# Kernel tuning notes

Hardware: AMD Instinct MI355X
Metric: run time of the kernel (lower is better)

## Reference

```python
import jax, jax.numpy as jnp
import numpy as np
from jax import lax

SCOPE = 15
RICKER_WIDTH = 3.0
DAMP = 0.12
MAX_STEPS = 10


def mexican_hat(scope, width, damping):
    # ricker / mexican-hat wavelet sampled at `scope` integer-spaced points, scaled by damping
    x = np.linspace(-(scope // 2), scope // 2, scope).astype(np.float32)
    norm = 2.0 / (np.sqrt(3.0 * width) * np.pi ** 0.25)
    w = damping * norm * (1.0 - (x / width) ** 2) * np.exp(-(x ** 2) / (2.0 * width ** 2))
    return jnp.asarray(w, dtype=jnp.float32)


def setup_inputs() -> dict:
    key = jax.random.key(0)
    activations = jax.random.normal(key, (32, 256, 56, 56), dtype=jnp.float32)
    w_rec = mexican_hat(SCOPE, RICKER_WIDTH, DAMP)  # [scope]
    return {"activations": activations, "w_rec": w_rec, "max_steps": MAX_STEPS}


def reference(activations, w_rec, max_steps):
    # activations: [B, C, H, W]; inhibition conv runs along the C axis only.
    scope = w_rec.shape[0]
    pad = scope // 2
    x = activations[:, None]                     # [B, 1, C, H, W]
    kernel = w_rec.reshape(1, 1, scope, 1, 1)    # OIDHW

    def conv(y):
        return lax.conv_general_dilated(
            y, kernel,
            window_strides=(1, 1, 1),
            padding=[(pad, pad), (0, 0), (0, 0)],
            dimension_numbers=("NCDHW", "OIDHW", "NCDHW"),
        )

    # fixed-point iteration: state <- activations + W_rec * state  (threshold=0 => always max_steps iters)
    state = x
    for _ in range(max_steps):
        state = x + conv(state)
    return state[:, 0]  # squeeze channel dim -> [B, C, H, W]
```

## Files before the change

kernel.cpp:

```cpp
#include <hip/hip_runtime.h>


#define NCH 256
#define PAD 7
#define SCOPE 15
#define SPATIAL 3136
#define PER_B 802816
#define STW 32
#define STILES_PER_B 98
#define NTILES 3136
#define GRID_APPLY 512
#define MAXCH 12
#define BUFW 8192

typedef __attribute__((ext_vector_type(8))) __bf16 bf16x8;
typedef __attribute__((ext_vector_type(16))) float float16;
typedef __attribute__((ext_vector_type(4))) unsigned int uint4v;
typedef __attribute__((ext_vector_type(2))) unsigned int uint2v;

static __device__ __forceinline__ unsigned short f2bf_rn_u(float f) {
  unsigned u = __builtin_bit_cast(unsigned int, f);
  return (unsigned short)((u + 0x7FFFu + ((u >> 16) & 1u)) >> 16);
}
static __device__ __forceinline__ float bf2f_u(unsigned short h) {
  unsigned u = ((unsigned)h) << 16;
  return __builtin_bit_cast(float, u);
}
static __device__ __forceinline__ unsigned pack_bf2(float a, float b) {
  return (unsigned)f2bf_rn_u(a) | ((unsigned)f2bf_rn_u(b) << 16);
}
static __device__ __forceinline__ void split2(float a, float b,
                                              unsigned& h, unsigned& l) {
  h = pack_bf2(a, b);
  const float ra = a - __builtin_bit_cast(float, h << 16);
  const float rb = b - __builtin_bit_cast(float, h & 0xFFFF0000u);
  l = pack_bf2(ra, rb);
}

__global__ void build_M_kernel(const float* __restrict__ w,
                               const int* __restrict__ max_steps_p,
                               unsigned short* __restrict__ Mh,
                               unsigned short* __restrict__ Ml) {
  const int d = blockIdx.x;
  const int c = threadIdx.x;
  __shared__ float v[2][NCH];
  __shared__ float wsh[SCOPE];
  if (c < SCOPE) wsh[c] = w[c];
  const float e = (c == d) ? 1.0f : 0.0f;
  v[0][c] = e;
  __syncthreads();
  const int steps = *max_steps_p;
  int cur = 0;
  for (int t = 0; t < steps; ++t) {
    float s = e;
#pragma unroll
    for (int j = 0; j < SCOPE; ++j) {
      const int cc = c + j - PAD;
      if (cc >= 0 && cc < NCH) s += wsh[j] * v[cur][cc];
    }
    cur ^= 1;
    v[cur][c] = s;
    __syncthreads();
  }
  const float f = v[cur][c];
  const unsigned short h = f2bf_rn_u(f);
  Mh[c * NCH + d] = h;
  Ml[c * NCH + d] = f2bf_rn_u(f - bf2f_u(h));
}

__global__ __launch_bounds__(512, 4) void apply_M_kernel(
    const float* __restrict__ x, const unsigned short* __restrict__ Mh,
    const unsigned short* __restrict__ Ml, float* __restrict__ out) {
  __shared__ unsigned XB[2 * BUFW];

  const int tid  = threadIdx.x;
  const int lane = tid & 63;
  const int w    = tid >> 6;
  const int m    = lane & 31;
  const int half = lane >> 5;
  const int c0   = w * 32;

  int clo = c0 - 70; if (clo < 0) clo = 0; clo >>= 4;
  int chi = c0 + 101; if (chi > 255) chi = 255; chi >>= 4;
  const int nch = chi - clo + 1;

  const unsigned short* mh = Mh + (c0 + m) * NCH + clo * 16 + half * 8;
  const unsigned short* ml = Ml + (c0 + m) * NCH + clo * 16 + half * 8;

  const int sq = (tid & 7) * 4;
  const int dg = tid >> 3;

  int tau = blockIdx.x;
  int bo = 0;
  float4 g0, g1, g2, g3;
  {
    const float* gb = x + (size_t)(tau / STILES_PER_B) * PER_B
                        + (size_t)(tau % STILES_PER_B) * STW;
    g0 = *(const float4*)(gb + (size_t)(2 * dg) * SPATIAL + sq);
    g1 = *(const float4*)(gb + (size_t)(2 * dg + 1) * SPATIAL + sq);
    g2 = *(const float4*)(gb + (size_t)(2 * dg + 128) * SPATIAL + sq);
    g3 = *(const float4*)(gb + (size_t)(2 * dg + 129) * SPATIAL + sq);
  }

#pragma unroll 1
  for (; tau < NTILES; tau += GRID_APPLY) {
    {
      unsigned h0, h1, h2, h3, l0, l1, l2, l3;
      split2(g0.x, g1.x, h0, l0); split2(g0.y, g1.y, h1, l1);
      split2(g0.z, g1.z, h2, l2); split2(g0.w, g1.w, h3, l3);
      unsigned* p = &XB[bo + dg * 64 + sq * 2];
      *(uint4v*)(p)     = (uint4v){h0, l0, h1, l1};
      *(uint4v*)(p + 4) = (uint4v){h2, l2, h3, l3};
      split2(g2.x, g3.x, h0, l0); split2(g2.y, g3.y, h1, l1);
      split2(g2.z, g3.z, h2, l2); split2(g2.w, g3.w, h3, l3);
      unsigned* q = &XB[bo + (dg + 64) * 64 + sq * 2];
      *(uint4v*)(q)     = (uint4v){h0, l0, h1, l1};
      *(uint4v*)(q + 4) = (uint4v){h2, l2, h3, l3};
    }

    const int ntau = tau + GRID_APPLY;
    if (ntau < NTILES) {
      const float* gb = x + (size_t)(ntau / STILES_PER_B) * PER_B
                          + (size_t)(ntau % STILES_PER_B) * STW;
      g0 = *(const float4*)(gb + (size_t)(2 * dg) * SPATIAL + sq);
      g1 = *(const float4*)(gb + (size_t)(2 * dg + 1) * SPATIAL + sq);
      g2 = *(const float4*)(gb + (size_t)(2 * dg + 128) * SPATIAL + sq);
      g3 = *(const float4*)(gb + (size_t)(2 * dg + 129) * SPATIAL + sq);
    }

    asm volatile("s_waitcnt lgkmcnt(0)" ::: "memory");
    __builtin_amdgcn_s_barrier();

    const unsigned short* mhp = mh;
    const unsigned short* mlp = ml;
    asm volatile("" : "+v"(mhp), "+v"(mlp));

    float16 a0, a1;
#pragma unroll
    for (int q = 0; q < 16; ++q) { a0[q] = 0.0f; a1[q] = 0.0f; }

    bf16x8 cAh = *(const bf16x8*)(mhp);
    bf16x8 cAl = *(const bf16x8*)(mlp);
#pragma unroll
    for (int i = 0; i < MAXCH; ++i) {
      if (i < nch) {
        bf16x8 nAh, nAl;
        if (i + 1 < nch) {
          nAh = *(const bf16x8*)(mhp + (i + 1) * 16);
          nAl = *(const bf16x8*)(mlp + (i + 1) * 16);
        }
        const int k2b = (clo + i) * 8 + half * 4;
        const unsigned* bp = &XB[bo + k2b * 64 + 2 * m];
        const uint2v r0 = *(const uint2v*)(bp);
        const uint2v r1 = *(const uint2v*)(bp + 64);
        const uint2v r2 = *(const uint2v*)(bp + 128);
        const uint2v r3 = *(const uint2v*)(bp + 192);
        const uint4v hw = {r0.x, r1.x, r2.x, r3.x};
        const uint4v lw = {r0.y, r1.y, r2.y, r3.y};
        const bf16x8 bh = __builtin_bit_cast(bf16x8, hw);
        const bf16x8 bl = __builtin_bit_cast(bf16x8, lw);
        a0 = __builtin_amdgcn_mfma_f32_32x32x16_bf16(cAh, bh, a0, 0, 0, 0);
        a1 = __builtin_amdgcn_mfma_f32_32x32x16_bf16(cAh, bl, a1, 0, 0, 0);
        a1 = __builtin_amdgcn_mfma_f32_32x32x16_bf16(cAl, bh, a1, 0, 0, 0);
        cAh = nAh; cAl = nAl;
      }
    }

    const int b  = tau / STILES_PER_B;
    const int s0 = (tau % STILES_PER_B) * STW;
    float* ob = out + (size_t)b * PER_B + (size_t)s0 + m;
#pragma unroll
    for (int r = 0; r < 16; ++r) {
      const int row = (r & 3) + 8 * (r >> 2) + 4 * half;
      ob[(size_t)(c0 + row) * SPATIAL] = a0[r] + a1[r];
    }

    bo ^= BUFW;
  }
}

extern "C" void kernel_launch(void* const* d_in, const int* in_sizes, int n_in,
                              void* d_out, int out_size, void* d_ws, size_t ws_size,
                              hipStream_t stream) {
  const float* x = (const float*)d_in[0];
  const float* w = (const float*)d_in[1];
  const int* ms = (const int*)d_in[2];
  float* out = (float*)d_out;

  unsigned short* Mh = (unsigned short*)d_ws;
  unsigned short* Ml = Mh + NCH * NCH;

  build_M_kernel<<<NCH, NCH, 0, stream>>>(w, ms, Mh, Ml);
  apply_M_kernel<<<GRID_APPLY, 512, 0, stream>>>(x, Mh, Ml, out);
}
```

Baseline: 249.2 us.

## Pre-swizzle banded M into MFMA fragment layout and launch one tile per block

The build kernel now writes the hi/lo bf16 parts of the propagation matrix directly in the per-wave MFMA A-fragment order, and only for the band each wave uses. Each lane can then fetch its operand with one contiguous 16-byte load. The apply kernel drops the persistent grid-stride loop with double-buffered LDS and register prefetch. It launches one block per spatial tile with a single LDS buffer and a higher occupancy hint. This trades explicit load/compute overlap for more resident blocks and simpler, coalesced matrix loads, and it adds per-block launch and prologue overhead.

Measured after the change: 208.4 us. 16.4% less time.

```diff
diff --git a/kernel.cpp b/kernel.cpp
--- a/kernel.cpp
+++ b/kernel.cpp
@@ -9,9 +9,7 @@
 #define STW 32
 #define STILES_PER_B 98
 #define NTILES 3136
-#define GRID_APPLY 512
 #define MAXCH 12
-#define BUFW 8192
 
 typedef __attribute__((ext_vector_type(8))) __bf16 bf16x8;
 typedef __attribute__((ext_vector_type(16))) float float16;
@@ -39,8 +37,8 @@
 
 __global__ void build_M_kernel(const float* __restrict__ w,
                                const int* __restrict__ max_steps_p,
-                               unsigned short* __restrict__ Mh,
-                               unsigned short* __restrict__ Ml) {
+                               unsigned short* __restrict__ AhF,
+                               unsigned short* __restrict__ AlF) {
   const int d = blockIdx.x;
   const int c = threadIdx.x;
   __shared__ float v[2][NCH];
@@ -64,14 +62,28 @@
   }
   const float f = v[cur][c];
   const unsigned short h = f2bf_rn_u(f);
-  Mh[c * NCH + d] = h;
-  Ml[c * NCH + d] = f2bf_rn_u(f - bf2f_u(h));
+  const unsigned short l = f2bf_rn_u(f - bf2f_u(h));
+
+  const int wv = c >> 5;
+  const int c0 = wv * 32;
+  int clo = c0 - 70; if (clo < 0) clo = 0; clo >>= 4;
+  int chi = c0 + 101; if (chi > 255) chi = 255; chi >>= 4;
+  const int ch = d >> 4;
+  if (ch >= clo && ch <= chi) {
+    const int i    = ch - clo;
+    const int half = (d >> 3) & 1;
+    const int j    = d & 7;
+    const int lane = half * 32 + (c & 31);
+    const size_t dst = ((size_t)(wv * MAXCH + i) * 64 + lane) * 8 + j;
+    AhF[dst] = h;
+    AlF[dst] = l;
+  }
 }
 
-__global__ __launch_bounds__(512, 4) void apply_M_kernel(
-    const float* __restrict__ x, const unsigned short* __restrict__ Mh,
-    const unsigned short* __restrict__ Ml, float* __restrict__ out) {
-  __shared__ unsigned XB[2 * BUFW];
+__global__ __launch_bounds__(512, 8) void apply_M_kernel(
+    const float* __restrict__ x, const unsigned short* __restrict__ AhF,
+    const unsigned short* __restrict__ AlF, float* __restrict__ out) {
+  __shared__ unsigned XB[8192];
 
   const int tid  = threadIdx.x;
   const int lane = tid & 63;
@@ -84,98 +96,68 @@
   int chi = c0 + 101; if (chi > 255) chi = 255; chi >>= 4;
   const int nch = chi - clo + 1;
 
-  const unsigned short* mh = Mh + (c0 + m) * NCH + clo * 16 + half * 8;
-  const unsigned short* ml = Ml + (c0 + m) * NCH + clo * 16 + half * 8;
-
   const int sq = (tid & 7) * 4;
   const int dg = tid >> 3;
 
-  int tau = blockIdx.x;
-  int bo = 0;
-  float4 g0, g1, g2, g3;
+  const int tau = blockIdx.x;
+  const float* gb = x + (size_t)(tau / STILES_PER_B) * PER_B
+                      + (size_t)(tau % STILES_PER_B) * STW;
+  const float4 g0 = *(const float4*)(gb + (size_t)(2 * dg) * SPATIAL + sq);
+  const float4 g1 = *(const float4*)(gb + (size_t)(2 * dg + 1) * SPATIAL + sq);
+  const float4 g2 = *(const float4*)(gb + (size_t)(2 * dg + 128) * SPATIAL + sq);
+  const float4 g3 = *(const float4*)(gb + (size_t)(2 * dg + 129) * SPATIAL + sq);
+
   {
-    const float* gb = x + (size_t)(tau / STILES_PER_B) * PER_B
-                        + (size_t)(tau % STILES_PER_B) * STW;
-    g0 = *(const float4*)(gb + (size_t)(2 * dg) * SPATIAL + sq);
-    g1 = *(const float4*)(gb + (size_t)(2 * dg + 1) * SPATIAL + sq);
-    g2 = *(const float4*)(gb + (size_t)(2 * dg + 128) * SPATIAL + sq);
-    g3 = *(const float4*)(gb + (size_t)(2 * dg + 129) * SPATIAL + sq);
+    unsigned h0, h1, h2, h3, l0, l1, l2, l3;
+    split2(g0.x, g1.x, h0, l0); split2(g0.y, g1.y, h1, l1);
+    split2(g0.z, g1.z, h2, l2); split2(g0.w, g1.w, h3, l3);
+    unsigned* p = &XB[dg * 64 + sq * 2];
+    *(uint4v*)(p)     = (uint4v){h0, l0, h1, l1};
+    *(uint4v*)(p + 4) = (uint4v){h2, l2, h3, l3};
+    split2(g2.x, g3.x, h0, l0); split2(g2.y, g3.y, h1, l1);
+    split2(g2.z, g3.z, h2, l2); split2(g2.w, g3.w, h3, l3);
+    unsigned* q = &XB[(dg + 64) * 64 + sq * 2];
+    *(uint4v*)(q)     = (uint4v){h0, l0, h1, l1};
+    *(uint4v*)(q + 4) = (uint4v){h2, l2, h3, l3};
+  }
+  __syncthreads();
+
+  const unsigned short* mhp = AhF + ((size_t)(w * MAXCH) * 64 + lane) * 8;
+  const unsigned short* mlp = AlF + ((size_t)(w * MAXCH) * 64 + lane) * 8;
+  asm volatile("" : "+v"(mhp), "+v"(mlp));
+
+  float16 a0, a1;
+#pragma unroll
+  for (int q = 0; q < 16; ++q) { a0[q] = 0.0f; a1[q] = 0.0f; }
+
+#pragma unroll
+  for (int i = 0; i < MAXCH; ++i) {
+    if (i < nch) {
+      const bf16x8 Ah = *(const bf16x8*)(mhp + i * 512);
+      const bf16x8 Al = *(const bf16x8*)(mlp + i * 512);
+      const int k2b = (clo + i) * 8 + half * 4;
+      const unsigned* bp = &XB[k2b * 64 + 2 * m];
+      const uint2v r0 = *(const uint2v*)(bp);
+      const uint2v r1 = *(const uint2v*)(bp + 64);
+      const uint2v r2 = *(const uint2v*)(bp + 128);
+      const uint2v r3 = *(const uint2v*)(bp + 192);
+      const uint4v hw = {r0.x, r1.x, r2.x, r3.x};
+      const uint4v lw = {r0.y, r1.y, r2.y, r3.y};
+      const bf16x8 bh = __builtin_bit_cast(bf16x8, hw);
+      const bf16x8 bl = __builtin_bit_cast(bf16x8, lw);
+      a0 = __builtin_amdgcn_mfma_f32_32x32x16_bf16(Ah, bh, a0, 0, 0, 0);
+      a1 = __builtin_amdgcn_mfma_f32_32x32x16_bf16(Ah, bl, a1, 0, 0, 0);
+      a1 = __builtin_amdgcn_mfma_f32_32x32x16_bf16(Al, bh, a1, 0, 0, 0);
+    }
   }
 
-#pragma unroll 1
-  for (; tau < NTILES; tau += GRID_APPLY) {
-    {
-      unsigned h0, h1, h2, h3, l0, l1, l2, l3;
-      split2(g0.x, g1.x, h0, l0); split2(g0.y, g1.y, h1, l1);
-      split2(g0.z, g1.z, h2, l2); split2(g0.w, g1.w, h3, l3);
-      unsigned* p = &XB[bo + dg * 64 + sq * 2];
-      *(uint4v*)(p)     = (uint4v){h0, l0, h1, l1};
-      *(uint4v*)(p + 4) = (uint4v){h2, l2, h3, l3};
-      split2(g2.x, g3.x, h0, l0); split2(g2.y, g3.y, h1, l1);
-      split2(g2.z, g3.z, h2, l2); split2(g2.w, g3.w, h3, l3);
-      unsigned* q = &XB[bo + (dg + 64) * 64 + sq * 2];
-      *(uint4v*)(q)     = (uint4v){h0, l0, h1, l1};
-      *(uint4v*)(q + 4) = (uint4v){h2, l2, h3, l3};
-    }
-
-    const int ntau = tau + GRID_APPLY;
-    if (ntau < NTILES) {
-      const float* gb = x + (size_t)(ntau / STILES_PER_B) * PER_B
-                          + (size_t)(ntau % STILES_PER_B) * STW;
-      g0 = *(const float4*)(gb + (size_t)(2 * dg) * SPATIAL + sq);
-      g1 = *(const float4*)(gb + (size_t)(2 * dg + 1) * SPATIAL + sq);
-      g2 = *(const float4*)(gb + (size_t)(2 * dg + 128) * SPATIAL + sq);
-      g3 = *(const float4*)(gb + (size_t)(2 * dg + 129) * SPATIAL + sq);
-    }
-
-    asm volatile("s_waitcnt lgkmcnt(0)" ::: "memory");
-    __builtin_amdgcn_s_barrier();
-
-    const unsigned short* mhp = mh;
-    const unsigned short* mlp = ml;
-    asm volatile("" : "+v"(mhp), "+v"(mlp));
-
-    float16 a0, a1;
+  const int b  = tau / STILES_PER_B;
+  const int s0 = (tau % STILES_PER_B) * STW;
+  float* ob = out + (size_t)b * PER_B + (size_t)s0 + m;
 #pragma unroll
-    for (int q = 0; q < 16; ++q) { a0[q] = 0.0f; a1[q] = 0.0f; }
-
-    bf16x8 cAh = *(const bf16x8*)(mhp);
-    bf16x8 cAl = *(const bf16x8*)(mlp);
-#pragma unroll
-    for (int i = 0; i < MAXCH; ++i) {
-      if (i < nch) {
-        bf16x8 nAh, nAl;
-        if (i + 1 < nch) {
-          nAh = *(const bf16x8*)(mhp + (i + 1) * 16);
-          nAl = *(const bf16x8*)(mlp + (i + 1) * 16);
-        }
-        const int k2b = (clo + i) * 8 + half * 4;
-        const unsigned* bp = &XB[bo + k2b * 64 + 2 * m];
-        const uint2v r0 = *(const uint2v*)(bp);
-        const uint2v r1 = *(const uint2v*)(bp + 64);
-        const uint2v r2 = *(const uint2v*)(bp + 128);
-        const uint2v r3 = *(const uint2v*)(bp + 192);
-        const uint4v hw = {r0.x, r1.x, r2.x, r3.x};
-        const uint4v lw = {r0.y, r1.y, r2.y, r3.y};
-        const bf16x8 bh = __builtin_bit_cast(bf16x8, hw);
-        const bf16x8 bl = __builtin_bit_cast(bf16x8, lw);
-        a0 = __builtin_amdgcn_mfma_f32_32x32x16_bf16(cAh, bh, a0, 0, 0, 0);
-        a1 = __builtin_amdgcn_mfma_f32_32x32x16_bf16(cAh, bl, a1, 0, 0, 0);
-        a1 = __builtin_amdgcn_mfma_f32_32x32x16_bf16(cAl, bh, a1, 0, 0, 0);
-        cAh = nAh; cAl = nAl;
-      }
-    }
-
-    const int b  = tau / STILES_PER_B;
-    const int s0 = (tau % STILES_PER_B) * STW;
-    float* ob = out + (size_t)b * PER_B + (size_t)s0 + m;
-#pragma unroll
-    for (int r = 0; r < 16; ++r) {
-      const int row = (r & 3) + 8 * (r >> 2) + 4 * half;
-      ob[(size_t)(c0 + row) * SPATIAL] = a0[r] + a1[r];
-    }
-
-    bo ^= BUFW;
+  for (int r = 0; r < 16; ++r) {
+    const int row = (r & 3) + 8 * (r >> 2) + 4 * half;
+    ob[(size_t)(c0 + row) * SPATIAL] = a0[r] + a1[r];
   }
 }
 
@@ -187,9 +169,9 @@
   const int* ms = (const int*)d_in[2];
   float* out = (float*)d_out;
 
-  unsigned short* Mh = (unsigned short*)d_ws;
-  unsigned short* Ml = Mh + NCH * NCH;
+  unsigned short* AhF = (unsigned short*)d_ws;
+  unsigned short* AlF = AhF + 8 * MAXCH * 64 * 8;
 
-  build_M_kernel<<<NCH, NCH, 0, stream>>>(w, ms, Mh, Ml);
-  apply_M_kernel<<<GRID_APPLY, 512, 0, stream>>>(x, Mh, Ml, out);
+  build_M_kernel<<<NCH, NCH, 0, stream>>>(w, ms, AhF, AlF);
+  apply_M_kernel<<<NTILES, 512, 0, stream>>>(x, AhF, AlF, out);
 }
```
